# Kernel optimization log

Hardware: AMD Instinct MI355X
Metric: run time of the kernel (lower is better)

## Reference

```python
import jax, jax.numpy as jnp
import numpy as np

NUM_GROUPS = 32
EPS = 1e-6

def group_norm(x, gamma, beta):
    # x: [B, C, P]
    B, C, P = x.shape
    xg = x.reshape(B, NUM_GROUPS, C // NUM_GROUPS, P)
    mean = jnp.mean(xg, axis=(2, 3), keepdims=True)
    var = jnp.var(xg, axis=(2, 3), keepdims=True)
    xn = ((xg - mean) * jax.lax.rsqrt(var + EPS)).reshape(B, C, P)
    return xn * gamma[None, :, None] + beta[None, :, None]

def conv1x1(h, w, b):
    # h: [B, C, P], w: [C_out, C_in], b: [C_out]
    return jnp.einsum('oc,bcp->bop', w, h) + b[None, :, None]

def setup_inputs() -> dict:
    key = jax.random.key(0)
    ks = jax.random.split(key, 10)
    B, C, P = 4, 512, 4096
    x = jax.random.normal(ks[0], (B, C, P), dtype=jnp.float32)
    gn_gamma = jnp.ones((C,), dtype=jnp.float32)
    gn_beta = jnp.zeros((C,), dtype=jnp.float32)
    s = 0.02
    wq = jax.random.normal(ks[1], (C, C), dtype=jnp.float32) * s
    bq = jax.random.normal(ks[2], (C,), dtype=jnp.float32) * s
    wk = jax.random.normal(ks[3], (C, C), dtype=jnp.float32) * s
    bk = jax.random.normal(ks[4], (C,), dtype=jnp.float32) * s
    wv = jax.random.normal(ks[5], (C, C), dtype=jnp.float32) * s
    bv = jax.random.normal(ks[6], (C,), dtype=jnp.float32) * s
    wo = jax.random.normal(ks[7], (C, C), dtype=jnp.float32) * s
    bo = jax.random.normal(ks[8], (C,), dtype=jnp.float32) * s
    return {"x": x, "gn_gamma": gn_gamma, "gn_beta": gn_beta,
            "wq": wq, "bq": bq, "wk": wk, "bk": bk,
            "wv": wv, "bv": bv, "wo": wo, "bo": bo}

def reference(x, gn_gamma, gn_beta, wq, bq, wk, bk, wv, bv, wo, bo):
    h = group_norm(x, gn_gamma, gn_beta)          # [B, C, P]
    q = conv1x1(h, wq, bq)                         # [B, C, P]
    k = conv1x1(h, wk, bk)                         # [B, C, P]
    v = conv1x1(h, wv, bv)                         # [B, C, P]
    C = q.shape[1]
    scale = 1.0 / jnp.sqrt(jnp.float32(C))
    # w[b, i, j] = sum_c q[b, c, i] * k[b, c, j]
    w = jnp.einsum('bci,bcj->bij', q, k) * scale   # [B, P, P]
    w = jax.nn.softmax(w, axis=2)
    # h_out[b, c, i] = sum_j v[b, c, j] * w[b, i, j]
    h = jnp.einsum('bij,bcj->bci', w, v)           # [B, C, P]
    h = conv1x1(h, wo, bo)
    return x + h
```

## Files before the change

kernel.cpp:

```cpp
#include <hip/hip_runtime.h>
#include <stdint.h>


typedef __bf16 bf16_t;
typedef __attribute__((ext_vector_type(4))) __bf16 bf16x4;
typedef __attribute__((ext_vector_type(8))) __bf16 bf16x8;
typedef __attribute__((ext_vector_type(4))) float floatx4;
typedef __attribute__((ext_vector_type(8))) int intx8;

constexpr int CDIM = 512;
constexpr int PDIM = 4096;

constexpr int ctz_c(int n) { return (n & 1) ? 0 : 1 + ctz_c(n >> 1); }

__device__ __forceinline__ void ld_g2l(const void* g, void* l) {
  __builtin_amdgcn_global_load_lds(
      (const __attribute__((address_space(1))) void*)g,
      (__attribute__((address_space(3))) void*)l,
      16, 0, 0);
}

__device__ __forceinline__ uint32_t pk_fp8x4(float a, float b, float c,
                                             float d) {
  int r = __builtin_amdgcn_cvt_pk_fp8_f32(a, b, 0, false);
  r = __builtin_amdgcn_cvt_pk_fp8_f32(c, d, r, true);
  return (uint32_t)r;
}

__device__ __forceinline__ intx8 ld_frag(const uint8_t* base, int s0,
                                         int s1) {
  union {
    uint4 u[2];
    intx8 v;
  } r;
  r.u[0] = *(const uint4*)(base + s0);
  r.u[1] = *(const uint4*)(base + s1);
  return r.v;
}

__device__ __forceinline__ int sigma_row(int r) {
  return (r & 64) + ((r & 15) << 2) + ((r >> 4) & 3);
}

template <int GX, int GY, int GZ>
__device__ __forceinline__ void xcd_remap(int& bx, int& by, int& bz) {
  constexpr int NWG = GX * GY * GZ;
  static_assert((NWG & 7) == 0 && (GX & (GX - 1)) == 0 &&
                    (GY & (GY - 1)) == 0,
                "pow2 grid, nwg%8==0");
  int lin = bx + GX * (by + GY * bz);
  int wg = (lin & 7) * (NWG >> 3) + (lin >> 3);
  bx = wg & (GX - 1);
  int t = wg >> ctz_c(GX);
  by = t & (GY - 1);
  bz = t >> ctz_c(GY);
}

enum { EPI_QK = 0, EPI_V = 1, EPI_OUT = 4, EPI_EXP = 2, EPI_PV = 5 };

template <int EPI, int TM, int NT, bool SWZ, int K, int LDA, int LDB,
          int LDC, int GX = 1, int GY = 1, int GZ = 1>
__global__ __launch_bounds__(NT) void gemm_tn(
    const bf16_t* __restrict__ A, const bf16_t* __restrict__ B, long sAb,
    long sBb, long sCb, void* __restrict__ Cv,
    const float* __restrict__ bias, const float* __restrict__ xres) {
  constexpr int NW = NT / 64;
  constexpr int WROWS = TM / (NW / 2);
  constexpr int MI = WROWS / 16;
  constexpr int RB = NT / 8;
  constexpr int AB = TM / RB;
  constexpr int BB = 128 / RB;
  constexpr int PMAX = AB > BB ? AB : BB;
  __shared__ bf16_t Asm[TM * 64];
  __shared__ bf16_t Bsm[128 * 64];

  const int tid = threadIdx.x;
  const int w = tid >> 6, l = tid & 63;
  int bx = blockIdx.x, by = blockIdx.y, bz = blockIdx.z;
  if constexpr (SWZ) xcd_remap<GX, GY, GZ>(bx, by, bz);
  const int m0 = by * TM, n0 = bx * 128;

  const bf16_t* Ab = A + (long)bz * sAb + (long)m0 * LDA;
  const bf16_t* Bb = B + (long)bz * sBb + (long)n0 * LDB;

  const int r0 = 8 * w + (l >> 3);
  const int schunk = (l & 7) ^ (l >> 3);
  const bf16_t* ga = Ab + (long)r0 * LDA + schunk * 8;
  const bf16_t* gb = Bb + schunk * 8;
  bf16_t* lA = Asm + (8 * w) * 64;
  bf16_t* lB = Bsm + (8 * w) * 64;

  const int wr = w >> 1, wc = w & 1;
  const int fr = l & 15, fq = l >> 4, l7 = l & 7;

  floatx4 acc[MI][4];
  floatx4 zz = {0.f, 0.f, 0.f, 0.f};
#pragma unroll
  for (int i = 0; i < MI; i++)
#pragma unroll
    for (int j = 0; j < 4; j++) acc[i][j] = zz;

#pragma unroll 8
  for (int it = 0; it < K / 64; it++) {
    const int kb = it * 64;
#pragma unroll
    for (int p = 0; p < PMAX; p++) {
      if (p < AB) ld_g2l(ga + (long)(p * RB) * LDA + kb, lA + p * RB * 64);
      if (p < BB) {
        const int sig = sigma_row(r0 + RB * p);
        ld_g2l(gb + (long)sig * LDB + kb, lB + p * RB * 64);
      }
    }
    __syncthreads();
#pragma unroll
    for (int ks = 0; ks < 2; ks++) {
      bf16x8 af[MI], bfv[4];
      const int ch = (ks * 4 + fq);
#pragma unroll
      for (int mi = 0; mi < MI; mi++) {
        int row = wr * WROWS + mi * 16 + fr;
        af[mi] = *(const bf16x8*)(Asm + row * 64 + ((ch ^ l7) * 8));
      }
#pragma unroll
      for (int ni = 0; ni < 4; ni++) {
        int row = wc * 64 + ni * 16 + fr;
        bfv[ni] = *(const bf16x8*)(Bsm + row * 64 + ((ch ^ l7) * 8));
      }
#pragma unroll
      for (int mi = 0; mi < MI; mi++)
#pragma unroll
        for (int ni = 0; ni < 4; ni++)
          acc[mi][ni] = __builtin_amdgcn_mfma_f32_16x16x32_bf16(
              af[mi], bfv[ni], acc[mi][ni], 0, 0, 0);
    }
    __syncthreads();
  }

  const int rb = fq * 4;
  const int gcolb = n0 + wc * 64 + 4 * fr;
#pragma unroll
  for (int mi = 0; mi < MI; mi++) {
#pragma unroll
    for (int i = 0; i < 4; i++) {
      const int grow = m0 + wr * WROWS + mi * 16 + rb + i;
      float v0 = acc[mi][0][i], v1 = acc[mi][1][i];
      float v2 = acc[mi][2][i], v3 = acc[mi][3][i];
      if constexpr (EPI == EPI_QK) {
        const float4 b4 = *(const float4*)(bias + gcolb);
        *(uint32_t*)((uint8_t*)Cv + (long)bz * sCb + (long)grow * LDC +
                     gcolb) =
            pk_fp8x4(v0 + b4.x, v1 + b4.y, v2 + b4.z, v3 + b4.w);
      } else if constexpr (EPI == EPI_V) {
        const float bb = bias[grow];
        uint32_t d = pk_fp8x4(v0 + bb, v1 + bb, v2 + bb, v3 + bb);
        *(uint32_t*)((uint8_t*)Cv + (long)bz * sCb + (long)grow * LDC +
                     gcolb) = d;
      } else {
        int ob = gcolb >> 12, op = gcolb & 4095;
        long o = ((long)ob * CDIM + grow) * PDIM + op;
        const float4 xr = *(const float4*)(xres + o);
        const float bb = bias[grow];
        float4 ov = {v0 + bb + xr.x, v1 + bb + xr.y, v2 + bb + xr.z,
                     v3 + bb + xr.w};
        *(float4*)((float*)Cv + o) = ov;
      }
    }
  }
}

template <int EPI, int TM, int SA, int NT, int K, int LDA, int LDB, int LDC,
          int GX, int GY, int GZ>
__global__ __launch_bounds__(NT) void gemm_f8(
    const uint8_t* __restrict__ A, const uint8_t* __restrict__ B, long sAb,
    long sBb, long sCb, void* __restrict__ Cv) {
  constexpr int NW = NT / 64;
  constexpr int WROWS = TM / (NW / 2);
  constexpr int MI = WROWS / 16;
  constexpr int RB = NT / 8;
  constexpr int AB = TM / RB;
  constexpr int BB = 128 / RB;
  constexpr int PMAX = AB > BB ? AB : BB;
  __shared__ uint8_t Asm[TM * 128];
  __shared__ uint8_t Bsm[128 * 128];

  const int tid = threadIdx.x;
  const int w = tid >> 6, l = tid & 63;
  int bx = blockIdx.x, by = blockIdx.y, bz = blockIdx.z;
  xcd_remap<GX, GY, GZ>(bx, by, bz);
  const int m0 = by * TM, n0 = bx * 128;

  const uint8_t* Ab = A + (long)bz * sAb + (long)m0 * LDA;
  const uint8_t* Bb = B + (long)bz * sBb + (long)n0 * LDB;

  const int r0 = 8 * w + (l >> 3);
  const int schunk = (l & 7) ^ (l >> 3);
  const uint8_t* ga = Ab + (long)r0 * LDA + schunk * 16;
  const uint8_t* gb = Bb + schunk * 16;
  uint8_t* lA = Asm + (8 * w) * 128;
  uint8_t* lB = Bsm + (8 * w) * 128;

  const int wr = w >> 1, wc = w & 1;
  const int fr = l & 15, fq = l >> 4, l7 = l & 7;

  floatx4 acc[MI][4];
  floatx4 accr[MI];
#pragma unroll
  for (int i = 0; i < MI; i++) {
#pragma unroll
    for (int j = 0; j < 4; j++) acc[i][j] = floatx4{0.f, 0.f, 0.f, 0.f};
    accr[i] = floatx4{0.f, 0.f, 0.f, 0.f};
  }

  const int s0 = ((2 * fq) ^ l7) * 16;
  const int s1 = ((2 * fq + 1) ^ l7) * 16;

#pragma unroll 1
  for (int it = 0; it < K / 128; it++) {
    const int kb = it * 128;
#pragma unroll
    for (int p = 0; p < PMAX; p++) {
      if (p < AB) ld_g2l(ga + (long)(p * RB) * LDA + kb, lA + p * RB * 128);
      if (p < BB) {
        const int sig = sigma_row(r0 + RB * p);
        ld_g2l(gb + (long)sig * LDB + kb, lB + p * RB * 128);
      }
    }
    __syncthreads();

    intx8 af[MI];
#pragma unroll
    for (int mi = 0; mi < MI; mi++)
      af[mi] = ld_frag(Asm + (wr * WROWS + mi * 16 + fr) * 128, s0, s1);
#pragma unroll
    for (int ni = 0; ni < 4; ni++) {
      intx8 bf = ld_frag(Bsm + (wc * 64 + ni * 16 + fr) * 128, s0, s1);
#pragma unroll
      for (int mi = 0; mi < MI; mi++)
        acc[mi][ni] = __builtin_amdgcn_mfma_scale_f32_16x16x128_f8f6f4(
            af[mi], bf, acc[mi][ni], 0, 0, 0, SA, 0, 127);
    }
    if constexpr (EPI == EPI_PV) {
      const int one8 = 0x38383838;
      const intx8 ones = {one8, one8, one8, one8, one8, one8, one8, one8};
#pragma unroll
      for (int mi = 0; mi < MI; mi++)
        accr[mi] = __builtin_amdgcn_mfma_scale_f32_16x16x128_f8f6f4(
            af[mi], ones, accr[mi], 0, 0, 0, SA, 0, 127);
    }
    __syncthreads();
  }

  const int rb = fq * 4;
  const int gcolb = n0 + wc * 64 + 4 * fr;
#pragma unroll
  for (int mi = 0; mi < MI; mi++) {
#pragma unroll
    for (int i = 0; i < 4; i++) {
      const int grow = m0 + wr * WROWS + mi * 16 + rb + i;
      if constexpr (EPI == EPI_EXP) {
        float p0 = exp2f(acc[mi][0][i]), p1 = exp2f(acc[mi][1][i]);
        float p2 = exp2f(acc[mi][2][i]), p3 = exp2f(acc[mi][3][i]);
        *(uint32_t*)((uint8_t*)Cv + (long)bz * sCb + (long)grow * LDC +
                     gcolb) = pk_fp8x4(p0, p1, p2, p3);
      } else {
        const float inv = __builtin_amdgcn_rcpf(accr[mi][i]);
        bf16x4 o = {(bf16_t)(acc[mi][0][i] * inv),
                    (bf16_t)(acc[mi][1][i] * inv),
                    (bf16_t)(acc[mi][2][i] * inv),
                    (bf16_t)(acc[mi][3][i] * inv)};
        *(bf16x4*)((bf16_t*)Cv + (long)bz * sCb + (long)grow * LDC + gcolb) =
            o;
      }
    }
  }
}

__global__ __launch_bounds__(256) void gn_stats(const float* __restrict__ x,
                                                float2* __restrict__ part) {
  const int i = blockIdx.x;
  const float4* xp = (const float4*)(x + (long)i * 8192);
  float s0 = 0.f, s1 = 0.f;
  for (int j = threadIdx.x; j < 2048; j += 256) {
    float4 v = xp[j];
    s0 += v.x + v.y + v.z + v.w;
    s1 += v.x * v.x + v.y * v.y + v.z * v.z + v.w * v.w;
  }
  for (int o = 32; o; o >>= 1) {
    s0 += __shfl_xor(s0, o);
    s1 += __shfl_xor(s1, o);
  }
  __shared__ float r0[4], r1[4];
  if ((threadIdx.x & 63) == 0) {
    r0[threadIdx.x >> 6] = s0;
    r1[threadIdx.x >> 6] = s1;
  }
  __syncthreads();
  if (threadIdx.x == 0)
    part[i] = make_float2(r0[0] + r0[1] + r0[2] + r0[3],
                          r1[0] + r1[1] + r1[2] + r1[3]);
}

__global__ __launch_bounds__(256) void gn_norm(
    const float* __restrict__ x, const float* __restrict__ gamma,
    const float* __restrict__ beta, const float2* __restrict__ part,
    bf16_t* __restrict__ h_t) {
  const int b = blockIdx.x >> 7;
  const int p0 = (blockIdx.x & 127) * 32;
  const int t = threadIdx.x;
  __shared__ float gmS[512], btS[512];
  __shared__ float gmean[32], grstd[32];
  __shared__ __align__(16) bf16_t tile[32 * 520];

  if (t < 32) {
    const float2* pp = part + (b * 32 + t) * 8;
    float s0 = 0.f, s1 = 0.f;
#pragma unroll
    for (int s = 0; s < 8; s++) {
      float2 v = pp[s];
      s0 += v.x;
      s1 += v.y;
    }
    float mean = s0 * (1.f / 65536.f);
    float var = s1 * (1.f / 65536.f) - mean * mean;
    gmean[t] = mean;
    grstd[t] = rsqrtf(var + 1e-6f);
  }
  __syncthreads();
  for (int c = t; c < 512; c += 256) {
    float g = gamma[c] * grstd[c >> 4];
    gmS[c] = g;
    btS[c] = beta[c] - gmean[c >> 4] * g;
  }
  __syncthreads();

  const int cc = t >> 3, pcol = (t & 7) * 4;
  for (int pass = 0; pass < 16; pass++) {
    int c = pass * 32 + cc;
    float4 v = *(const float4*)(x + ((long)(b * 512 + c)) * 4096 + p0 + pcol);
    float g = gmS[c], bb = btS[c];
    tile[(pcol + 0) * 520 + c] = (bf16_t)(v.x * g + bb);
    tile[(pcol + 1) * 520 + c] = (bf16_t)(v.y * g + bb);
    tile[(pcol + 2) * 520 + c] = (bf16_t)(v.z * g + bb);
    tile[(pcol + 3) * 520 + c] = (bf16_t)(v.w * g + bb);
  }
  __syncthreads();
  const int p = t >> 3;
  bf16_t* orow = h_t + ((long)(b * 4096 + p0 + p)) * 512;
  const bf16_t* trow = tile + p * 520;
#pragma unroll
  for (int j = 0; j < 8; j++) {
    int ch = (t & 7) + 8 * j;
    *(uint4*)(orow + ch * 8) = *(const uint4*)(trow + ch * 8);
  }
}

__global__ __launch_bounds__(256) void cvt_weights(
    const float* __restrict__ wq, const float* __restrict__ wk,
    const float* __restrict__ wv, const float* __restrict__ wo,
    const float* __restrict__ bq, const float* __restrict__ bk,
    bf16_t* __restrict__ out, float* __restrict__ bqk) {
  constexpr float QW = 1.02013936f;
  int i = blockIdx.x * 256 + threadIdx.x;
  out[i] = (bf16_t)(wq[i] * QW);
  out[262144 + i] = (bf16_t)wk[i];
  out[2 * 262144 + i] = (bf16_t)wv[i];
  out[3 * 262144 + i] = (bf16_t)wo[i];
  if (i < 512)
    bqk[i] = bq[i] * QW;
  else if (i < 1024)
    bqk[i] = bk[i - 512];
}

extern "C" void kernel_launch(void* const* d_in, const int* in_sizes, int n_in,
                              void* d_out, int out_size, void* d_ws,
                              size_t ws_size, hipStream_t stream) {
  const float* x = (const float*)d_in[0];
  const float* gamma = (const float*)d_in[1];
  const float* beta = (const float*)d_in[2];
  const float* wq = (const float*)d_in[3];
  const float* bq = (const float*)d_in[4];
  const float* wk = (const float*)d_in[5];
  const float* bk = (const float*)d_in[6];
  const float* wv = (const float*)d_in[7];
  const float* bv = (const float*)d_in[8];
  const float* wo = (const float*)d_in[9];
  const float* bo = (const float*)d_in[10];

  char* ws = (char*)d_ws;
  bf16_t* h_t = (bf16_t*)(ws);
  uint8_t* qk8 = (uint8_t*)(ws + (16l << 20));
  uint8_t* v_c = (uint8_t*)(ws + (48l << 20));
  bf16_t* h_at = (bf16_t*)(ws + (64l << 20));
  bf16_t* w_b = (bf16_t*)(ws + (80l << 20));
  float2* part = (float2*)(ws + (83l << 20));
  float* bqk = (float*)(ws + (83l << 20) + (64l << 10));
  uint8_t* Sbuf = (uint8_t*)(ws + (84l << 20));

  const long sQK8 = (long)PDIM * 1024;
  const long sS = (long)PDIM * PDIM;

  cvt_weights<<<1024, 256, 0, stream>>>(wq, wk, wv, wo, bq, bk, w_b, bqk);
  gn_stats<<<1024, 256, 0, stream>>>(x, part);
  gn_norm<<<512, 256, 0, stream>>>(x, gamma, beta, part, h_t);
  gemm_tn<EPI_QK, 128, 256, true, 512, 512, 512, 1024, 8, 128, 1>
      <<<dim3(8, 128, 1), 256, 0, stream>>>(h_t, w_b, 0, 0, 0, qk8, bqk,
                                            nullptr);
  gemm_tn<EPI_V, 64, 256, false, 512, 512, 512, 16384>
      <<<dim3(128, 8, 1), 256, 0, stream>>>(w_b + 2 * 262144, h_t, 0, 0, 0,
                                            v_c, bv, nullptr);
  gemm_f8<EPI_EXP, 128, 123, 256, 512, 1024, 1024, 4096, 32, 32, 4>
      <<<dim3(32, 32, 4), 256, 0, stream>>>(qk8, qk8 + 512, sQK8, sQK8, sS,
                                            Sbuf);
  gemm_f8<EPI_PV, 128, 127, 256, 4096, 4096, 16384, 512, 4, 32, 4>
      <<<dim3(4, 32, 4), 256, 0, stream>>>(Sbuf, v_c, sS, 4096,
                                           (long)PDIM * CDIM, h_at);
  gemm_tn<EPI_OUT, 64, 256, false, 512, 512, 512, 4096>
      <<<dim3(128, 8, 1), 256, 0, stream>>>(w_b + 3 * 262144, h_at, 0, 0, 0,
                                            d_out, bo, x);
}
```

Baseline: 254.2 us.

## Double-buffer LDS tiles in fp8 GEMM to overlap loads with MFMA

Splits the shared-memory A and B tiles into two buffers and restructures the K loop as a ping-pong. The global-to-LDS load for the next K slice is issued before the MFMA work on the current slice, so memory latency can hide behind compute. The cost is twice the LDS footprint, which may lower occupancy, and the K iteration count must be even.

```diff
diff --git a/kernel.cpp b/kernel.cpp
--- a/kernel.cpp
+++ b/kernel.cpp
@@ -180,8 +180,10 @@
   constexpr int AB = TM / RB;
   constexpr int BB = 128 / RB;
   constexpr int PMAX = AB > BB ? AB : BB;
-  __shared__ uint8_t Asm[TM * 128];
-  __shared__ uint8_t Bsm[128 * 128];
+  constexpr int NITER = K / 128;
+  static_assert((NITER & 1) == 0, "ping-pong needs even iter count");
+  __shared__ uint8_t Asm[2][TM * 128];
+  __shared__ uint8_t Bsm[2][128 * 128];
 
   const int tid = threadIdx.x;
   const int w = tid >> 6, l = tid & 63;
@@ -196,8 +198,7 @@
   const int schunk = (l & 7) ^ (l >> 3);
   const uint8_t* ga = Ab + (long)r0 * LDA + schunk * 16;
   const uint8_t* gb = Bb + schunk * 16;
-  uint8_t* lA = Asm + (8 * w) * 128;
-  uint8_t* lB = Bsm + (8 * w) * 128;
+  const int lofs = (8 * w) * 128;
 
   const int wr = w >> 1, wc = w & 1;
   const int fr = l & 15, fq = l >> 4, l7 = l & 7;
@@ -214,26 +215,26 @@
   const int s0 = ((2 * fq) ^ l7) * 16;
   const int s1 = ((2 * fq + 1) ^ l7) * 16;
 
-#pragma unroll 1
-  for (int it = 0; it < K / 128; it++) {
-    const int kb = it * 128;
+  auto stage = [&](int buf, int kb) {
 #pragma unroll
     for (int p = 0; p < PMAX; p++) {
-      if (p < AB) ld_g2l(ga + (long)(p * RB) * LDA + kb, lA + p * RB * 128);
+      if (p < AB)
+        ld_g2l(ga + (long)(p * RB) * LDA + kb, &Asm[buf][lofs + p * RB * 128]);
       if (p < BB) {
         const int sig = sigma_row(r0 + RB * p);
-        ld_g2l(gb + (long)sig * LDB + kb, lB + p * RB * 128);
-      }
-    }
-    __syncthreads();
-
+        ld_g2l(gb + (long)sig * LDB + kb, &Bsm[buf][lofs + p * RB * 128]);
+      }
+    }
+  };
+  auto compute = [&](int buf) {
     intx8 af[MI];
 #pragma unroll
     for (int mi = 0; mi < MI; mi++)
-      af[mi] = ld_frag(Asm + (wr * WROWS + mi * 16 + fr) * 128, s0, s1);
+      af[mi] =
+          ld_frag(&Asm[buf][(wr * WROWS + mi * 16 + fr) * 128], s0, s1);
 #pragma unroll
     for (int ni = 0; ni < 4; ni++) {
-      intx8 bf = ld_frag(Bsm + (wc * 64 + ni * 16 + fr) * 128, s0, s1);
+      intx8 bf = ld_frag(&Bsm[buf][(wc * 64 + ni * 16 + fr) * 128], s0, s1);
 #pragma unroll
       for (int mi = 0; mi < MI; mi++)
         acc[mi][ni] = __builtin_amdgcn_mfma_scale_f32_16x16x128_f8f6f4(
@@ -247,6 +248,17 @@
         accr[mi] = __builtin_amdgcn_mfma_scale_f32_16x16x128_f8f6f4(
             af[mi], ones, accr[mi], 0, 0, 0, SA, 0, 127);
     }
+  };
+
+  stage(0, 0);
+  __syncthreads();
+#pragma unroll 1
+  for (int it = 0; it < NITER; it += 2) {
+    stage(1, (it + 1) * 128);
+    compute(0);
+    __syncthreads();
+    if (it + 2 < NITER) stage(0, (it + 2) * 128);
+    compute(1);
     __syncthreads();
   }
 
```

Result: no change. 249.6 us (-1.8%).
